# Kernel tuning notes

Measured on AMD Instinct MI355X. Metric: run time of the kernel, lower is better.

The kernel has to match this reference:

```python
import jax, jax.numpy as jnp
import numpy as np

M_COMP = 8      # number of output components m (n = m * tmax)
TMAX = 512
BS = 32
N = M_COMP * TMAX  # 4096


def setup_inputs() -> dict:
    key = jax.random.key(0)
    k1, k2, k3, k4 = jax.random.split(key, 4)
    # K must be symmetric positive definite for the Cholesky factorization.
    A = jax.random.normal(k1, (N, N), dtype=jnp.float32)
    K = A @ A.T / N + 1e-2 * jnp.eye(N, dtype=jnp.float32)
    # Sigma: diagonal measurement-noise covariance (positive diagonal).
    Sigma = jnp.diag(jax.random.uniform(k2, (N,), dtype=jnp.float32, minval=0.1, maxval=0.5))
    mu = jax.random.normal(k3, (N,), dtype=jnp.float32)
    Y = jax.random.normal(k4, (BS * N,), dtype=jnp.float32)
    return {"Y": Y, "mu": mu, "K": K, "Sigma": Sigma, "bs": BS, "tmax": TMAX}


def reference(Y, mu, K, Sigma, bs, tmax):
    n = mu.shape[0]  # m * tmax
    KS = K + Sigma
    # Chol_inv: inv = L^{-T} L^{-1} = (K + Sigma)^{-1}
    L = jnp.linalg.cholesky(KS)
    Linv = jnp.linalg.inv(L)
    inv = Linv.T @ Linv  # [n, n]
    # Block-diagonal quadratic form == sum of per-trajectory quadratic forms.
    diff = mu[None, :] - Y.reshape(bs, n)  # [bs, n]
    quad = jnp.einsum('bi,ij,bj->', diff, inv, diff)
    # log det(K + Sigma); slogdet is the stable equivalent (det > 0 for SPD).
    _, logdet = jnp.linalg.slogdet(KS)
    lml = (-quad / (2.0 * bs)
           - 0.5 * logdet
           - 0.5 * tmax * jnp.log(jnp.asarray(2.0 * np.pi, dtype=KS.dtype)))
    return -lml
```

## Files before the change

kernel.cpp:

```cpp
#include <hip/hip_runtime.h>
#include <math.h>

#define Nn 4096
#define BSc 32
#define NB 128
#define NBP 132
#define NBB 32
#define NBLK 33
#define NK 32
#define TILE_ELEMS (NB * NB)
#define NTILES 561

#define SM_DINV 67584
#define SM_SIZE 67712

typedef float f32x4 __attribute__((ext_vector_type(4)));
typedef short bf16x8 __attribute__((ext_vector_type(8)));

__device__ __forceinline__ size_t tile_off(int i, int j) {
  return ((size_t)(j * NBLK - (j * (j - 1)) / 2 + (i - j))) * TILE_ELEMS;
}

__device__ __forceinline__ unsigned short f2bf(float f) {
  union { float f; unsigned int u; } v; v.f = f;
  unsigned int r = v.u + 0x7fffu + ((v.u >> 16) & 1u);
  return (unsigned short)(r >> 16);
}
__device__ __forceinline__ float bf2f(unsigned short b) {
  union { unsigned int u; float f; } v; v.u = ((unsigned int)b) << 16;
  return v.f;
}

__global__ __launch_bounds__(256) void prep(const float* __restrict__ Y,
                                            const float* __restrict__ mu,
                                            const float* __restrict__ Kp,
                                            const float* __restrict__ Sg,
                                            float* __restrict__ W) {
  int bid = blockIdx.x;
  int j = 0;
  while (j + 1 < NBLK) {
    int nxt = (j + 1) * NBLK - ((j + 1) * j) / 2;
    if (bid < nxt) break;
    ++j;
  }
  int start = j * NBLK - (j * (j - 1)) / 2;
  int i = j + (bid - start);
  float* T = W + tile_off(i, j);
  int tid = threadIdx.x;
  for (int idx = tid; idx < TILE_ELEMS; idx += 256) {
    int li = idx >> 7, lj = idx & 127;
    int gr = i * NB + li, gc = j * NB + lj;
    float v = 0.0f;
    if (gr < Nn) {
      v = Kp[(size_t)gr * Nn + gc];
      if (gr == gc) v += Sg[(size_t)gr * Nn + gr];
    } else {
      int b = gr - Nn;
      if (b < BSc && gc < Nn) v = mu[gc] - Y[(size_t)b * Nn + gc];
    }
    T[idx] = v;
  }
}

__device__ __forceinline__ void factor_lds(float (*T)[NBP], float* dinv_sh,
                                           int tid) {
  int lane = tid & 63, wid = tid >> 6;
#pragma unroll 1
  for (int kb = 0; kb < 4; ++kb) {
    int o = kb * NBB;
    if (wid == 0) {
      int ii = lane & 31;
      float cc[NBB];
#pragma unroll
      for (int p = 0; p < NBB; ++p) cc[p] = T[o + ii][o + p];
#pragma unroll
      for (int j = 0; j < NBB; ++j) {
        float s = cc[j];
#pragma unroll
        for (int p = 0; p < NBB; ++p) {
          if (p < j) s -= cc[p] * __shfl(cc[p], j, 64);
        }
        float sj = __shfl(s, j, 64);
        float d = sqrtf(sj);
        if (ii == j) cc[j] = d;
        else if (ii > j) cc[j] = s / d;
      }
      if (lane < 32) {
#pragma unroll
        for (int p = 0; p < NBB; ++p) {
          if (p <= ii) T[o + ii][o + p] = cc[p];
        }
      }
    }
    __syncthreads();
    if (tid < NBB) dinv_sh[tid] = 1.0f / T[o + tid][o + tid];
    __syncthreads();
    int R = NB - o - NBB;
    if (R > 0) {
      if (tid < R) {
        int r = o + NBB + tid;
        float x[NBB];
#pragma unroll
        for (int p4 = 0; p4 < 8; ++p4) {
          float4 v = *(const float4*)&T[r][o + p4 * 4];
          x[p4 * 4] = v.x; x[p4 * 4 + 1] = v.y; x[p4 * 4 + 2] = v.z; x[p4 * 4 + 3] = v.w;
        }
#pragma unroll
        for (int j = 0; j < NBB; ++j) {
          float s = x[j];
#pragma unroll
          for (int p = 0; p < NBB; ++p) {
            if (p < j) s -= x[p] * T[o + j][o + p];
          }
          x[j] = s * dinv_sh[j];
        }
#pragma unroll
        for (int c4 = 0; c4 < 8; ++c4) {
          float4 w; w.x = x[c4 * 4]; w.y = x[c4 * 4 + 1]; w.z = x[c4 * 4 + 2]; w.w = x[c4 * 4 + 3];
          *(float4*)&T[r][o + c4 * 4] = w;
        }
      }
      __syncthreads();
      int TL = R >> 2;
      int ntile = TL * (TL + 1) / 2;
#pragma unroll 1
      for (int t = tid; t < ntile; t += 256) {
        int ti = (int)((sqrtf(8.0f * t + 1.0f) - 1.0f) * 0.5f);
        while ((ti + 1) * (ti + 2) / 2 <= t) ++ti;
        while (ti * (ti + 1) / 2 > t) --ti;
        int tj = t - ti * (ti + 1) / 2;
        int tr = o + NBB + ti * 4, tc = o + NBB + tj * 4;
        float acc[4][4];
#pragma unroll
        for (int m = 0; m < 4; ++m)
#pragma unroll
          for (int n = 0; n < 4; ++n) acc[m][n] = 0.0f;
#pragma unroll
        for (int p4 = 0; p4 < 8; ++p4) {
          float4 a[4], b[4];
#pragma unroll
          for (int m = 0; m < 4; ++m) a[m] = *(const float4*)&T[tr + m][o + p4 * 4];
#pragma unroll
          for (int n = 0; n < 4; ++n) b[n] = *(const float4*)&T[tc + n][o + p4 * 4];
#pragma unroll
          for (int m = 0; m < 4; ++m)
#pragma unroll
            for (int n = 0; n < 4; ++n)
              acc[m][n] += a[m].x * b[n].x + a[m].y * b[n].y + a[m].z * b[n].z + a[m].w * b[n].w;
        }
#pragma unroll
        for (int m = 0; m < 4; ++m)
#pragma unroll
          for (int n = 0; n < 4; ++n) T[tr + m][tc + n] -= acc[m][n];
      }
    }
    __syncthreads();
  }
}

__global__ __launch_bounds__(256) void potf2(float* __restrict__ W, int k) {
  __shared__ __align__(16) unsigned char SMEM[SM_SIZE];
  float (*T)[NBP] = (float (*)[NBP])SMEM;
  float* dinv_sh = (float*)(SMEM + SM_DINV);
  float* G = W + tile_off(k, k);
  int tid = threadIdx.x;
  for (int idx = tid; idx < TILE_ELEMS / 4; idx += 256) {
    float4 v = ((const float4*)G)[idx];
    int r = idx >> 5, c = (idx & 31) * 4;
    *(float4*)&T[r][c] = v;
  }
  __syncthreads();
  factor_lds(T, dinv_sh, tid);
  for (int idx = tid; idx < TILE_ELEMS; idx += 256) {
    int i = idx >> 7, j = idx & 127;
    if (j <= i) G[idx] = T[i][j];
  }
}

__global__ __launch_bounds__(256) void trsm(float* __restrict__ W,
                                            unsigned short* __restrict__ PH,
                                            unsigned short* __restrict__ PL,
                                            int k) {
  __shared__ float Td[NB][NBP];
  __shared__ float X[NB][NBP];
  __shared__ float dinv_sh[NB];
  int tid = threadIdx.x;
  int i = k + 1 + blockIdx.x;
  int rows = (i == NBLK - 1) ? BSc : NB;
  const float* Gd = W + tile_off(k, k);
  const float* Gx = W + tile_off(i, k);
  for (int idx = tid; idx < TILE_ELEMS / 4; idx += 256) {
    float4 v = ((const float4*)Gd)[idx];
    float4 u = ((const float4*)Gx)[idx];
    int r = idx >> 5, c = (idx & 31) * 4;
    *(float4*)&Td[r][c] = v;
    if (r >= rows) { u.x = 0.0f; u.y = 0.0f; u.z = 0.0f; u.w = 0.0f; }
    *(float4*)&X[r][c] = u;
  }
  __syncthreads();
  if (tid < NB) dinv_sh[tid] = 1.0f / Td[tid][tid];
  __syncthreads();
  int rtile = (tid >> 3) * 4;
  int ctile = (tid & 7) * 4;
#pragma unroll 1
  for (int jb = 0; jb < 4; ++jb) {
    int o = jb * NBB;
    if (jb > 0) {
      float acc[4][4];
#pragma unroll
      for (int m = 0; m < 4; ++m)
#pragma unroll
        for (int n = 0; n < 4; ++n) acc[m][n] = 0.0f;
#pragma unroll 1
      for (int p4 = 0; p4 < (o >> 2); ++p4) {
        float4 a[4], b[4];
#pragma unroll
        for (int m = 0; m < 4; ++m) a[m] = *(const float4*)&X[rtile + m][p4 * 4];
#pragma unroll
        for (int n = 0; n < 4; ++n) b[n] = *(const float4*)&Td[o + ctile + n][p4 * 4];
#pragma unroll
        for (int m = 0; m < 4; ++m)
#pragma unroll
          for (int n = 0; n < 4; ++n)
            acc[m][n] += a[m].x * b[n].x + a[m].y * b[n].y + a[m].z * b[n].z + a[m].w * b[n].w;
      }
#pragma unroll
      for (int m = 0; m < 4; ++m)
#pragma unroll
        for (int n = 0; n < 4; ++n) X[rtile + m][o + ctile + n] -= acc[m][n];
      __syncthreads();
    }
    if (tid < NB) {
      int r = tid;
      float x[NBB];
#pragma unroll
      for (int p4 = 0; p4 < 8; ++p4) {
        float4 v = *(const float4*)&X[r][o + p4 * 4];
        x[p4 * 4] = v.x; x[p4 * 4 + 1] = v.y; x[p4 * 4 + 2] = v.z; x[p4 * 4 + 3] = v.w;
      }
#pragma unroll
      for (int j = 0; j < NBB; ++j) {
        float s = x[j];
#pragma unroll
        for (int p = 0; p < NBB; ++p) {
          if (p < j) s -= x[p] * Td[o + j][o + p];
        }
        x[j] = s * dinv_sh[o + j];
      }
#pragma unroll
      for (int c4 = 0; c4 < 8; ++c4) {
        float4 w; w.x = x[c4 * 4]; w.y = x[c4 * 4 + 1]; w.z = x[c4 * 4 + 2]; w.w = x[c4 * 4 + 3];
        *(float4*)&X[r][o + c4 * 4] = w;
      }
    }
    __syncthreads();
  }
  int r = tid >> 1, hf = tid & 1;
  unsigned short* ph = PH + (size_t)i * TILE_ELEMS + (size_t)r * NB + hf * 64;
  unsigned short* pl = PL + (size_t)i * TILE_ELEMS + (size_t)r * NB + hf * 64;
#pragma unroll 1
  for (int ch = 0; ch < 8; ++ch) {
    unsigned short hb[8], lb[8];
#pragma unroll
    for (int e = 0; e < 8; ++e) {
      float v = X[r][hf * 64 + ch * 8 + e];
      unsigned short h = f2bf(v);
      hb[e] = h;
      lb[e] = f2bf(v - bf2f(h));
    }
    *reinterpret_cast<uint4*>(&ph[ch * 8]) = *reinterpret_cast<const uint4*>(hb);
    *reinterpret_cast<uint4*>(&pl[ch * 8]) = *reinterpret_cast<const uint4*>(lb);
  }
}

__global__ __launch_bounds__(256) void syrk(const unsigned short* __restrict__ PH,
                                            const unsigned short* __restrict__ PL,
                                            float* __restrict__ W, int k) {
  int i = k + 1 + blockIdx.x, j = k + 1 + blockIdx.y;
  if (i < j) return;
  __shared__ __align__(16) unsigned char SMEM[SM_SIZE];
  unsigned short (*Ah)[40] = (unsigned short (*)[40])(SMEM);
  unsigned short (*Al)[40] = (unsigned short (*)[40])(SMEM + 10240);
  unsigned short (*Bh)[40] = (unsigned short (*)[40])(SMEM + 20480);
  unsigned short (*Bl)[40] = (unsigned short (*)[40])(SMEM + 30720);
  const unsigned short* Ahg = PH + (size_t)i * TILE_ELEMS;
  const unsigned short* Alg = PL + (size_t)i * TILE_ELEMS;
  const unsigned short* Bhg = PH + (size_t)j * TILE_ELEMS;
  const unsigned short* Blg = PL + (size_t)j * TILE_ELEMS;
  float* C = W + tile_off(i, j);
  int tid = threadIdx.x, lane = tid & 63, wid = tid >> 6;
  int wr = wid >> 1, wc = wid & 1, lm = lane & 15, lk = lane >> 4;
  f32x4 acc[4][4];
#pragma unroll
  for (int m = 0; m < 4; ++m)
#pragma unroll
    for (int n = 0; n < 4; ++n) acc[m][n] = (f32x4)0.0f;
  int r = tid >> 1, hf = tid & 1;
#pragma unroll 1
  for (int kb = 0; kb < 4; ++kb) {
    int kbase = kb * 32;
    if (kb) __syncthreads();
#pragma unroll
    for (int c = 0; c < 2; ++c) {
      int lc = (hf * 2 + c) * 8;
      int kc = kbase + lc;
      *reinterpret_cast<uint4*>(&Ah[r][lc]) = *reinterpret_cast<const uint4*>(&Ahg[(size_t)r * NB + kc]);
      *reinterpret_cast<uint4*>(&Al[r][lc]) = *reinterpret_cast<const uint4*>(&Alg[(size_t)r * NB + kc]);
      *reinterpret_cast<uint4*>(&Bh[r][lc]) = *reinterpret_cast<const uint4*>(&Bhg[(size_t)r * NB + kc]);
      *reinterpret_cast<uint4*>(&Bl[r][lc]) = *reinterpret_cast<const uint4*>(&Blg[(size_t)r * NB + kc]);
    }
    __syncthreads();
    bf16x8 ah[4], al[4], bh[4], bl[4];
#pragma unroll
    for (int mt = 0; mt < 4; ++mt) {
      int row = wr * 64 + mt * 16 + lm;
      ah[mt] = *reinterpret_cast<const bf16x8*>(&Ah[row][lk * 8]);
      al[mt] = *reinterpret_cast<const bf16x8*>(&Al[row][lk * 8]);
    }
#pragma unroll
    for (int nt = 0; nt < 4; ++nt) {
      int col = wc * 64 + nt * 16 + lm;
      bh[nt] = *reinterpret_cast<const bf16x8*>(&Bh[col][lk * 8]);
      bl[nt] = *reinterpret_cast<const bf16x8*>(&Bl[col][lk * 8]);
    }
#pragma unroll
    for (int mt = 0; mt < 4; ++mt)
#pragma unroll
      for (int nt = 0; nt < 4; ++nt) {
        acc[mt][nt] = __builtin_amdgcn_mfma_f32_16x16x32_bf16(ah[mt], bh[nt], acc[mt][nt], 0, 0, 0);
        acc[mt][nt] = __builtin_amdgcn_mfma_f32_16x16x32_bf16(al[mt], bh[nt], acc[mt][nt], 0, 0, 0);
        acc[mt][nt] = __builtin_amdgcn_mfma_f32_16x16x32_bf16(ah[mt], bl[nt], acc[mt][nt], 0, 0, 0);
      }
  }
  bool dofac = (blockIdx.x == 0 && blockIdx.y == 0 && i < NBLK - 1);
  if (!dofac) {
#pragma unroll
    for (int mt = 0; mt < 4; ++mt)
#pragma unroll
      for (int nt = 0; nt < 4; ++nt) {
#pragma unroll
        for (int q = 0; q < 4; ++q) {
          int rr = wr * 64 + mt * 16 + lk * 4 + q;
          int cc = wc * 64 + nt * 16 + lm;
          C[rr * NB + cc] -= acc[mt][nt][q];
        }
      }
  } else {
    __syncthreads();
    float (*T)[NBP] = (float (*)[NBP])SMEM;
    float* dinv_sh = (float*)(SMEM + SM_DINV);
    for (int idx = tid; idx < TILE_ELEMS / 4; idx += 256) {
      float4 v = ((const float4*)C)[idx];
      int rr = idx >> 5, cc = (idx & 31) * 4;
      *(float4*)&T[rr][cc] = v;
    }
    __syncthreads();
#pragma unroll
    for (int mt = 0; mt < 4; ++mt)
#pragma unroll
      for (int nt = 0; nt < 4; ++nt) {
#pragma unroll
        for (int q = 0; q < 4; ++q) {
          int rr = wr * 64 + mt * 16 + lk * 4 + q;
          int cc = wc * 64 + nt * 16 + lm;
          T[rr][cc] -= acc[mt][nt][q];
        }
      }
    __syncthreads();
    factor_lds(T, dinv_sh, tid);
    for (int idx = tid; idx < TILE_ELEMS; idx += 256) {
      int rr = idx >> 7, cc = idx & 127;
      if (cc <= rr) C[idx] = T[rr][cc];
    }
  }
}

__global__ __launch_bounds__(256) void finalize(const float* __restrict__ W,
                                                const int* __restrict__ bsp,
                                                const int* __restrict__ tmaxp,
                                                float* __restrict__ out) {
  __shared__ float rl[4], rq[4];
  int tid = threadIdx.x;
  float lsum = 0.0f;
  for (int d = tid; d < Nn; d += 256) {
    int db = d >> 7, dl = d & 127;
    lsum += logf(W[tile_off(db, db) + (size_t)dl * NB + dl]);
  }
  float qsum = 0.0f;
  if (tid < BSc) qsum = W[tile_off(NBLK - 1, NBLK - 1) + (size_t)tid * NB + tid];
  for (int o = 32; o > 0; o >>= 1) {
    lsum += __shfl_down(lsum, o, 64);
    qsum += __shfl_down(qsum, o, 64);
  }
  int lane = tid & 63, wid = tid >> 6;
  if (lane == 0) { rl[wid] = lsum; rq[wid] = qsum; }
  __syncthreads();
  if (tid == 0) {
    float Lt = rl[0] + rl[1] + rl[2] + rl[3];
    float Qt = rq[0] + rq[1] + rq[2] + rq[3];
    float bsf = (float)bsp[0];
    float tmaxf = (float)tmaxp[0];
    out[0] = -Qt / (2.0f * bsf) + Lt + 0.5f * tmaxf * logf(6.283185307179586f);
  }
}

extern "C" void kernel_launch(void* const* d_in, const int* in_sizes, int n_in,
                              void* d_out, int out_size, void* d_ws, size_t ws_size,
                              hipStream_t stream) {
  const float* Y   = (const float*)d_in[0];
  const float* mu  = (const float*)d_in[1];
  const float* Kp  = (const float*)d_in[2];
  const float* Sg  = (const float*)d_in[3];
  const int*   bsp = (const int*)d_in[4];
  const int*   tmp_= (const int*)d_in[5];
  float* W = (float*)d_ws;
  unsigned short* PH = (unsigned short*)(W + (size_t)NTILES * TILE_ELEMS);
  unsigned short* PL = PH + (size_t)NBLK * TILE_ELEMS;
  float* out = (float*)d_out;

  prep<<<NTILES, 256, 0, stream>>>(Y, mu, Kp, Sg, W);
  potf2<<<1, 256, 0, stream>>>(W, 0);

  for (int k = 0; k < NK; ++k) {
    int T = NBLK - (k + 1);
    trsm<<<T, 256, 0, stream>>>(W, PH, PL, k);
    dim3 g(T, T);
    syrk<<<g, 256, 0, stream>>>(PH, PL, W, k);
  }
  finalize<<<1, 256, 0, stream>>>(W, bsp, tmp_, out);
}
```

Baseline: 3.696 ms.

## Replace diagonal-block triangular solves with explicit inverse multiplies

Each 32x32 diagonal Cholesky sub-block is now inverted explicitly by the factoring wavefront using shuffles. The inverse is stored in LDS scratch and in a global buffer. Both the in-tile panel update and the trsm kernel then apply it as a dense matrix-vector product instead of a serial forward substitution with per-element dependency chains. This trades the latency-bound substitution for extra work in the factor kernel plus a global write and read of the inverse blocks. It also risks some numerical error from explicit inversion.

```diff
diff --git a/kernel.cpp b/kernel.cpp
--- a/kernel.cpp
+++ b/kernel.cpp
@@ -11,8 +11,7 @@
 #define TILE_ELEMS (NB * NB)
 #define NTILES 561
 
-#define SM_DINV 67584
-#define SM_SIZE 67712
+#define SM_SIZE 67584
 
 typedef float f32x4 __attribute__((ext_vector_type(4)));
 typedef short bf16x8 __attribute__((ext_vector_type(8)));
@@ -62,8 +61,8 @@
   }
 }
 
-__device__ __forceinline__ void factor_lds(float (*T)[NBP], float* dinv_sh,
-                                           int tid) {
+__device__ __forceinline__ void factor_lds(float (*T)[NBP],
+                                           float* __restrict__ Uinv, int tid) {
   int lane = tid & 63, wid = tid >> 6;
 #pragma unroll 1
   for (int kb = 0; kb < 4; ++kb) {
@@ -91,32 +90,58 @@
           if (p <= ii) T[o + ii][o + p] = cc[p];
         }
       }
-    }
-    __syncthreads();
-    if (tid < NBB) dinv_sh[tid] = 1.0f / T[o + tid][o + tid];
+      float v[NBB];
+#pragma unroll
+      for (int p = 0; p < NBB; ++p) v[p] = (p == ii) ? 1.0f : 0.0f;
+#pragma unroll
+      for (int q = 0; q < NBB; ++q) {
+        if (ii == q) {
+          float dq = 1.0f / cc[q];
+#pragma unroll
+          for (int p = 0; p < NBB; ++p) v[p] *= dq;
+        }
+#pragma unroll
+        for (int p = 0; p < NBB; ++p) {
+          float vq = __shfl(v[p], q, 64);
+          if (ii > q) v[p] -= cc[q] * vq;
+        }
+      }
+      if (lane < 32) {
+#pragma unroll
+        for (int p4 = 0; p4 < 8; ++p4) {
+          float4 w; w.x = v[p4 * 4]; w.y = v[p4 * 4 + 1];
+          w.z = v[p4 * 4 + 2]; w.w = v[p4 * 4 + 3];
+          *(float4*)&Uinv[kb * 1024 + ii * NBB + p4 * 4] = w;
+        }
+        if (kb < 3) {
+#pragma unroll
+          for (int p = 0; p < NBB; ++p) T[o + ii][o + NBB + p] = v[p];
+        }
+      }
+    }
     __syncthreads();
     int R = NB - o - NBB;
     if (R > 0) {
       if (tid < R) {
         int r = o + NBB + tid;
-        float x[NBB];
-#pragma unroll
-        for (int p4 = 0; p4 < 8; ++p4) {
-          float4 v = *(const float4*)&T[r][o + p4 * 4];
-          x[p4 * 4] = v.x; x[p4 * 4 + 1] = v.y; x[p4 * 4 + 2] = v.z; x[p4 * 4 + 3] = v.w;
-        }
-#pragma unroll
-        for (int j = 0; j < NBB; ++j) {
-          float s = x[j];
-#pragma unroll
-          for (int p = 0; p < NBB; ++p) {
-            if (p < j) s -= x[p] * T[o + j][o + p];
+        float4 xo4[8];
+#pragma unroll
+        for (int p4 = 0; p4 < 8; ++p4) xo4[p4] = *(const float4*)&T[r][o + p4 * 4];
+        float xn[NBB];
+#pragma unroll
+        for (int c = 0; c < NBB; ++c) {
+          float s = 0.0f;
+#pragma unroll
+          for (int p4 = 0; p4 < 8; ++p4) {
+            float4 u4 = *(const float4*)&T[o + c][o + NBB + p4 * 4];
+            s += xo4[p4].x * u4.x + xo4[p4].y * u4.y + xo4[p4].z * u4.z + xo4[p4].w * u4.w;
           }
-          x[j] = s * dinv_sh[j];
+          xn[c] = s;
         }
 #pragma unroll
         for (int c4 = 0; c4 < 8; ++c4) {
-          float4 w; w.x = x[c4 * 4]; w.y = x[c4 * 4 + 1]; w.z = x[c4 * 4 + 2]; w.w = x[c4 * 4 + 3];
+          float4 w; w.x = xn[c4 * 4]; w.y = xn[c4 * 4 + 1];
+          w.z = xn[c4 * 4 + 2]; w.w = xn[c4 * 4 + 3];
           *(float4*)&T[r][o + c4 * 4] = w;
         }
       }
@@ -158,10 +183,10 @@
   }
 }
 
-__global__ __launch_bounds__(256) void potf2(float* __restrict__ W, int k) {
+__global__ __launch_bounds__(256) void potf2(float* __restrict__ W,
+                                             float* __restrict__ Uinv, int k) {
   __shared__ __align__(16) unsigned char SMEM[SM_SIZE];
   float (*T)[NBP] = (float (*)[NBP])SMEM;
-  float* dinv_sh = (float*)(SMEM + SM_DINV);
   float* G = W + tile_off(k, k);
   int tid = threadIdx.x;
   for (int idx = tid; idx < TILE_ELEMS / 4; idx += 256) {
@@ -170,7 +195,7 @@
     *(float4*)&T[r][c] = v;
   }
   __syncthreads();
-  factor_lds(T, dinv_sh, tid);
+  factor_lds(T, Uinv, tid);
   for (int idx = tid; idx < TILE_ELEMS; idx += 256) {
     int i = idx >> 7, j = idx & 127;
     if (j <= i) G[idx] = T[i][j];
@@ -178,12 +203,13 @@
 }
 
 __global__ __launch_bounds__(256) void trsm(float* __restrict__ W,
+                                            const float* __restrict__ Uinv,
                                             unsigned short* __restrict__ PH,
                                             unsigned short* __restrict__ PL,
                                             int k) {
   __shared__ float Td[NB][NBP];
   __shared__ float X[NB][NBP];
-  __shared__ float dinv_sh[NB];
+  __shared__ float Uin[4][NBB][NBB + 4];
   int tid = threadIdx.x;
   int i = k + 1 + blockIdx.x;
   int rows = (i == NBLK - 1) ? BSc : NB;
@@ -197,8 +223,12 @@
     if (r >= rows) { u.x = 0.0f; u.y = 0.0f; u.z = 0.0f; u.w = 0.0f; }
     *(float4*)&X[r][c] = u;
   }
-  __syncthreads();
-  if (tid < NB) dinv_sh[tid] = 1.0f / Td[tid][tid];
+  for (int v4 = tid; v4 < 1024; v4 += 256) {
+    float4 u = *(const float4*)&Uinv[v4 * 4];
+    int kb = v4 >> 8, rem = v4 & 255;
+    int r = rem >> 3, c4 = rem & 7;
+    *(float4*)&Uin[kb][r][c4 * 4] = u;
+  }
   __syncthreads();
   int rtile = (tid >> 3) * 4;
   int ctile = (tid & 7) * 4;
@@ -232,24 +262,24 @@
     }
     if (tid < NB) {
       int r = tid;
-      float x[NBB];
-#pragma unroll
-      for (int p4 = 0; p4 < 8; ++p4) {
-        float4 v = *(const float4*)&X[r][o + p4 * 4];
-        x[p4 * 4] = v.x; x[p4 * 4 + 1] = v.y; x[p4 * 4 + 2] = v.z; x[p4 * 4 + 3] = v.w;
-      }
-#pragma unroll
-      for (int j = 0; j < NBB; ++j) {
-        float s = x[j];
-#pragma unroll
-        for (int p = 0; p < NBB; ++p) {
-          if (p < j) s -= x[p] * Td[o + j][o + p];
-        }
-        x[j] = s * dinv_sh[o + j];
+      float4 xo4[8];
+#pragma unroll
+      for (int p4 = 0; p4 < 8; ++p4) xo4[p4] = *(const float4*)&X[r][o + p4 * 4];
+      float xn[NBB];
+#pragma unroll
+      for (int c = 0; c < NBB; ++c) {
+        float s = 0.0f;
+#pragma unroll
+        for (int p4 = 0; p4 < 8; ++p4) {
+          float4 u4 = *(const float4*)&Uin[jb][c][p4 * 4];
+          s += xo4[p4].x * u4.x + xo4[p4].y * u4.y + xo4[p4].z * u4.z + xo4[p4].w * u4.w;
+        }
+        xn[c] = s;
       }
 #pragma unroll
       for (int c4 = 0; c4 < 8; ++c4) {
-        float4 w; w.x = x[c4 * 4]; w.y = x[c4 * 4 + 1]; w.z = x[c4 * 4 + 2]; w.w = x[c4 * 4 + 3];
+        float4 w; w.x = xn[c4 * 4]; w.y = xn[c4 * 4 + 1];
+        w.z = xn[c4 * 4 + 2]; w.w = xn[c4 * 4 + 3];
         *(float4*)&X[r][o + c4 * 4] = w;
       }
     }
@@ -275,7 +305,8 @@
 
 __global__ __launch_bounds__(256) void syrk(const unsigned short* __restrict__ PH,
                                             const unsigned short* __restrict__ PL,
-                                            float* __restrict__ W, int k) {
+                                            float* __restrict__ W,
+                                            float* __restrict__ Uinv, int k) {
   int i = k + 1 + blockIdx.x, j = k + 1 + blockIdx.y;
   if (i < j) return;
   __shared__ __align__(16) unsigned char SMEM[SM_SIZE];
@@ -348,7 +379,6 @@
   } else {
     __syncthreads();
     float (*T)[NBP] = (float (*)[NBP])SMEM;
-    float* dinv_sh = (float*)(SMEM + SM_DINV);
     for (int idx = tid; idx < TILE_ELEMS / 4; idx += 256) {
       float4 v = ((const float4*)C)[idx];
       int rr = idx >> 5, cc = (idx & 31) * 4;
@@ -367,7 +397,7 @@
         }
       }
     __syncthreads();
-    factor_lds(T, dinv_sh, tid);
+    factor_lds(T, Uinv, tid);
     for (int idx = tid; idx < TILE_ELEMS; idx += 256) {
       int rr = idx >> 7, cc = idx & 127;
       if (cc <= rr) C[idx] = T[rr][cc];
@@ -416,16 +446,17 @@
   float* W = (float*)d_ws;
   unsigned short* PH = (unsigned short*)(W + (size_t)NTILES * TILE_ELEMS);
   unsigned short* PL = PH + (size_t)NBLK * TILE_ELEMS;
+  float* Uinv = (float*)(PL + (size_t)NBLK * TILE_ELEMS);
   float* out = (float*)d_out;
 
   prep<<<NTILES, 256, 0, stream>>>(Y, mu, Kp, Sg, W);
-  potf2<<<1, 256, 0, stream>>>(W, 0);
+  potf2<<<1, 256, 0, stream>>>(W, Uinv, 0);
 
   for (int k = 0; k < NK; ++k) {
     int T = NBLK - (k + 1);
-    trsm<<<T, 256, 0, stream>>>(W, PH, PL, k);
+    trsm<<<T, 256, 0, stream>>>(W, Uinv, PH, PL, k);
     dim3 g(T, T);
-    syrk<<<g, 256, 0, stream>>>(PH, PL, W, k);
+    syrk<<<g, 256, 0, stream>>>(PH, PL, W, Uinv, k);
   }
   finalize<<<1, 256, 0, stream>>>(W, bsp, tmp_, out);
 }
```

After: 7.298 ms. 97.5% more time.
